# Performance work log

Measured on AMD Instinct MI355X. Metric: run time of the kernel, lower is better.

## Reference

```python
import jax, jax.numpy as jnp
import numpy as np

K_TOP = 2  # n_experts_per_tok
W_SCALE = 0.02  # keep activations numerically tame


def setup_inputs() -> dict:
    key = jax.random.key(0)
    ks = jax.random.split(key, 8)
    D, F, E = 1024, 1024, 8
    B, T = 4, 2048
    x = jax.random.normal(ks[0], (B, T, D), dtype=jnp.float32)
    router_w = jax.random.normal(ks[1], (D, E), dtype=jnp.float32) * W_SCALE
    sg = jax.random.normal(ks[2], (D, F), dtype=jnp.float32) * W_SCALE
    su = jax.random.normal(ks[3], (D, F), dtype=jnp.float32) * W_SCALE
    sd = jax.random.normal(ks[4], (F, D), dtype=jnp.float32) * W_SCALE
    wg = jax.random.normal(ks[5], (E, D, F), dtype=jnp.float32) * W_SCALE
    wu = jax.random.normal(ks[6], (E, D, F), dtype=jnp.float32) * W_SCALE
    wd = jax.random.normal(ks[7], (E, F, D), dtype=jnp.float32) * W_SCALE
    return {"x": x, "router_w": router_w, "sg": sg, "su": su, "sd": sd,
            "wg": wg, "wu": wu, "wd": wd}


def reference(x, router_w, sg, su, sd, wg, wu, wd):
    B, T, D = x.shape
    E = wg.shape[0]
    flat = x.reshape(-1, D)                       # [N, D]
    N = flat.shape[0]

    # shared SwiGLU expert (n_shared_experts = 1)
    shared = (jax.nn.silu(flat @ sg) * (flat @ su)) @ sd  # [N, D]

    # top-k softmax router with renormalization
    probs = jax.nn.softmax(flat @ router_w, axis=-1)      # [N, E]
    topk_p, topk_i = jax.lax.top_k(probs, K_TOP)          # [N, K]
    topk_p = topk_p / (jnp.sum(topk_p, axis=-1, keepdims=True) + 1e-9)

    # dense combine weights: scatter renormalized probs into [N, E]
    cw = jnp.zeros((N, E), dtype=flat.dtype).at[
        jnp.arange(N)[:, None], topk_i].add(topk_p)

    # per-expert SwiGLU on all tokens, weighted combine (jit-friendly MoE form)
    h = jax.nn.silu(jnp.einsum('nd,edf->nef', flat, wg)) \
        * jnp.einsum('nd,edf->nef', flat, wu)             # [N, E, F]
    eo = jnp.einsum('nef,efd->ned', h, wd)                # [N, E, D]
    routed = jnp.einsum('ned,ne->nd', eo, cw)             # [N, D]

    return (shared + routed).reshape(B, T, D)
```

## Files before the change

### kernel.cpp

```cpp
#include <hip/hip_runtime.h>

#define N_TOK    8192
#define D_DIM    1024
#define F_DIM    1024
#define NESH     9
#define MAX_RTD  18432
#define MAX_ROWS 26624
#define BM 256
#define BK 64
#define NK 16

#define MO 16
#define MT 25

typedef float  f4    __attribute__((ext_vector_type(4)));
typedef float  f32x4 __attribute__((ext_vector_type(4)));
typedef short  s16x8 __attribute__((ext_vector_type(8)));
typedef unsigned short u16x8 __attribute__((ext_vector_type(8)));
typedef unsigned short u16x4 __attribute__((ext_vector_type(4)));

static __device__ __forceinline__ unsigned short f2bf(float f) {
    union { float f; unsigned u; } v; v.f = f;
    unsigned r = v.u + 0x7FFFu + ((v.u >> 16) & 1u);
    return (unsigned short)(r >> 16);
}
static __device__ __forceinline__ float bf2f(unsigned short u) {
    union { unsigned u; float f; } v; v.u = ((unsigned)u) << 16; return v.f;
}

#define GLDS(gp, lp) __builtin_amdgcn_global_load_lds( \
    (const __attribute__((address_space(1))) void*)(gp), \
    (__attribute__((address_space(3))) void*)(lp), 16, 0, 0)

#define RSWZ(row, idx) ((idx) ^ (((row) & 7) << 3))

__global__ __launch_bounds__(256) void k_transpose(
    const float* __restrict__ wg, const float* __restrict__ wu,
    const float* __restrict__ wd, const float* __restrict__ sg,
    const float* __restrict__ su, const float* __restrict__ sd,
    unsigned short* __restrict__ wgt, unsigned short* __restrict__ wut,
    unsigned short* __restrict__ wdt)
{
    int bx = blockIdx.x;
    int m = bx >> 8;
    int tile = bx & 255;
    int ty = tile >> 4, tx = tile & 15;
    int set = m / 9, e = m % 9;
    const float* src; unsigned short* dst;
    if (set == 0)      { src = (e < 8) ? wg + (size_t)e*1048576 : sg; dst = wgt + (size_t)e*1048576; }
    else if (set == 1) { src = (e < 8) ? wu + (size_t)e*1048576 : su; dst = wut + (size_t)e*1048576; }
    else               { src = (e < 8) ? wd + (size_t)e*1048576 : sd; dst = wdt + (size_t)e*1048576; }

    __shared__ unsigned short ts[64 * 67];
    int t = threadIdx.x;
    int rT0 = ty * 64, cT0 = tx * 64;
    #pragma unroll
    for (int i = 0; i < 4; i++) {
        int idx = t + i * 256;
        int a  = idx >> 4;
        int b4 = (idx & 15) * 4;
        f4 v = *(const f4*)(src + (size_t)(cT0 + a) * 1024 + rT0 + b4);
        ts[a * 67 + b4 + 0] = f2bf(v[0]);
        ts[a * 67 + b4 + 1] = f2bf(v[1]);
        ts[a * 67 + b4 + 2] = f2bf(v[2]);
        ts[a * 67 + b4 + 3] = f2bf(v[3]);
    }
    __syncthreads();
    #pragma unroll
    for (int i = 0; i < 2; i++) {
        int slot = t + i * 256;
        int r  = slot >> 3;
        int c8 = (slot & 7) * 8;
        u16x8 o;
        #pragma unroll
        for (int k = 0; k < 8; k++) o[k] = ts[(c8 + k) * 67 + r];
        *(u16x8*)&dst[(size_t)(rT0 + r) * 1024 + cT0 + c8] = o;
    }
}

__global__ __launch_bounds__(256) void k_router(
    const float* __restrict__ x, const float* __restrict__ rw,
    unsigned short* __restrict__ xb,
    int* __restrict__ tk_i, float* __restrict__ tk_w)
{
    int wid = threadIdx.x >> 6, lane = threadIdx.x & 63;
    int n = blockIdx.x * 4 + wid;
    const float* xr = x + (size_t)n * D_DIM;
    unsigned short* xbr = xb + (size_t)n * D_DIM;
    float acc[8] = {0,0,0,0,0,0,0,0};
    #pragma unroll
    for (int it = 0; it < 4; it++) {
        int d0 = it * 256 + lane * 4;
        f4 xv = *(const f4*)(xr + d0);
        #pragma unroll
        for (int j = 0; j < 4; j++) {
            f4 r0 = *(const f4*)(rw + (size_t)(d0 + j) * 8);
            f4 r1 = *(const f4*)(rw + (size_t)(d0 + j) * 8 + 4);
            acc[0] += xv[j]*r0[0]; acc[1] += xv[j]*r0[1]; acc[2] += xv[j]*r0[2]; acc[3] += xv[j]*r0[3];
            acc[4] += xv[j]*r1[0]; acc[5] += xv[j]*r1[1]; acc[6] += xv[j]*r1[2]; acc[7] += xv[j]*r1[3];
        }
        u16x4 o; o[0]=f2bf(xv[0]); o[1]=f2bf(xv[1]); o[2]=f2bf(xv[2]); o[3]=f2bf(xv[3]);
        *(u16x4*)&xbr[d0] = o;
    }
    #pragma unroll
    for (int e = 0; e < 8; e++)
        for (int off = 32; off; off >>= 1)
            acc[e] += __shfl_xor(acc[e], off, 64);
    if (lane == 0) {
        float mx = acc[0];
        for (int e = 1; e < 8; e++) mx = fmaxf(mx, acc[e]);
        float p[8], s = 0.f;
        for (int e = 0; e < 8; e++) { p[e] = expf(acc[e] - mx); s += p[e]; }
        int i0 = 0;
        for (int e = 1; e < 8; e++) if (p[e] > p[i0]) i0 = e;
        int i1 = (i0 == 0) ? 1 : 0;
        for (int e = 0; e < 8; e++) if (e != i0 && p[e] > p[i1]) i1 = e;
        float p0 = p[i0] / s, p1 = p[i1] / s;
        float rs = p0 + p1 + 1e-9f;
        tk_i[2*n] = i0;  tk_i[2*n+1] = i1;
        tk_w[2*n] = p0 / rs;  tk_w[2*n+1] = p1 / rs;
    }
}

__global__ __launch_bounds__(1024) void k_count_scatter(
    const int* __restrict__ tk_i, const float* __restrict__ tk_w,
    int* __restrict__ meta,
    int* __restrict__ row_token, int* __restrict__ row_expert,
    int* __restrict__ tok_pos)
{
    __shared__ int cnt[1024 * 9];
    __shared__ int tot[8];
    __shared__ int off[9];
    const int t = threadIdx.x;
    const int lane = t & 63;
    const int wid = t >> 6;

    #pragma unroll
    for (int e = 0; e < 8; e++) cnt[t * 9 + e] = 0;
    __syncthreads();

    #pragma unroll
    for (int j = 0; j < 8; j++) {
        int n = t * 8 + j;
        cnt[t * 9 + tk_i[2 * n]]++;
        cnt[t * 9 + tk_i[2 * n + 1]]++;
    }
    __syncthreads();

    if (wid < 8) {
        const int e = wid;
        int carry = 0;
        for (int c = 0; c < 16; c++) {
            int i = c * 64 + lane;
            int v = cnt[i * 9 + e];
            int s = v;
            #pragma unroll
            for (int d = 1; d < 64; d <<= 1) {
                int u = __shfl_up(s, d, 64);
                if (lane >= d) s += u;
            }
            cnt[i * 9 + e] = s - v + carry;
            carry += __shfl(s, 63, 64);
        }
        if (lane == 0) tot[e] = carry;
    }
    __syncthreads();

    if (t == 0) {
        int acc = 0;
        #pragma unroll
        for (int e = 0; e < 8; e++) {
            off[e] = acc;
            meta[MO + e] = acc;
            acc += ((tot[e] + 255) >> 8) << 8;
        }
        off[8] = acc;
        meta[MO + 8] = acc;
        meta[MT] = acc + N_TOK;
    }
    __syncthreads();

    #pragma unroll
    for (int j = 0; j < 8; j++) {
        int n = t * 8 + j;
        #pragma unroll
        for (int k = 0; k < 2; k++) {
            int e = tk_i[2 * n + k];
            int pos = off[e] + cnt[t * 9 + e];
            cnt[t * 9 + e] = cnt[t * 9 + e] + 1;
            row_token[pos] = n; row_expert[pos] = e;
            tok_pos[2 * n + k] = pos;
        }
        int ps = off[8] + n;
        row_token[ps] = n; row_expert[ps] = 8;
    }
    #pragma unroll
    for (int e = 0; e < 8; e++) {
        int start = off[e] + tot[e], end = off[e + 1];
        for (int i = start + t; i < end; i += 1024) row_token[i] = -1;
    }
}

__global__ __launch_bounds__(512, 2) void k_gemm1(
    const unsigned short* __restrict__ xb,
    const unsigned short* __restrict__ wgt,
    const unsigned short* __restrict__ wut,
    const int* __restrict__ row_token,
    const int* __restrict__ row_expert,
    const int* __restrict__ meta,
    unsigned short* __restrict__ h)
{
    const int total = meta[MT];
    const int orig = blockIdx.x;
    const int bid = (orig & 7) * 104 + (orig >> 3);
    const int rt = bid >> 3, ct = bid & 7;
    const int row0 = rt * BM;
    if (row0 >= total) return;
    const int e = row_expert[row0];

    __shared__ __align__(16) unsigned short sA[2 * BM * BK];
    __shared__ __align__(16) unsigned short sBg[3 * 128 * BK];
    __shared__ __align__(16) unsigned short sBu[3 * 128 * BK];

    const int t = threadIdx.x;
    const int lane = t & 63;
    const int wid = t >> 6;
    const int wr = wid >> 1, wc = wid & 1;

    const unsigned short* asrc[4];
    #pragma unroll
    for (int i = 0; i < 4; i++) {
        int slot = t + i * 512;
        int row = slot >> 3;
        int cg  = (slot & 7) ^ (row & 7);
        int tok = row_token[row0 + row];
        if (tok < 0) tok = 0;
        asrc[i] = xb + (size_t)tok * D_DIM + cg * 8;
    }
    const unsigned short* bsrcg[2];
    const unsigned short* bsrcu[2];
    #pragma unroll
    for (int i = 0; i < 2; i++) {
        int slot = t + i * 512;
        int row = slot >> 3;
        int cg  = (slot & 7) ^ (row & 7);
        size_t off = ((size_t)e * F_DIM + ct * 128 + row) * D_DIM + cg * 8;
        bsrcg[i] = wgt + off;
        bsrcu[i] = wut + off;
    }

    f32x4 accg[4][4] = {}, accu[4][4] = {};

#define STAGE_A1(bb, k0) do { \
    unsigned short* dA = &sA[(bb) * (BM * BK)]; \
    _Pragma("unroll") \
    for (int i_ = 0; i_ < 4; i_++) GLDS(asrc[i_] + (k0), &dA[(t + i_ * 512) * 8]); \
    } while (0)
#define STAGE_B1(ss, k0) do { \
    unsigned short* dBg = &sBg[(ss) * (128 * BK)]; \
    unsigned short* dBu = &sBu[(ss) * (128 * BK)]; \
    _Pragma("unroll") \
    for (int i_ = 0; i_ < 2; i_++) { \
        GLDS(bsrcg[i_] + (k0), &dBg[(t + i_ * 512) * 8]); \
        GLDS(bsrcu[i_] + (k0), &dBu[(t + i_ * 512) * 8]); \
    } } while (0)

#define COMPUTE1(bb, ss) do { \
    const unsigned short* pA  = &sA[(bb) * (BM * BK)]; \
    const unsigned short* pBg = &sBg[(ss) * (128 * BK)]; \
    const unsigned short* pBu = &sBu[(ss) * (128 * BK)]; \
    _Pragma("unroll") \
    for (int kk = 0; kk < BK; kk += 32) { \
        const int koff = kk + (lane >> 4) * 8; \
        s16x8 a_[4], bg_[4], bu_[4]; \
        _Pragma("unroll") \
        for (int m_ = 0; m_ < 4; m_++) { \
            int row = wr * 64 + m_ * 16 + (lane & 15); \
            a_[m_] = *(const s16x8*)&pA[RSWZ(row, row * BK + koff)]; } \
        _Pragma("unroll") \
        for (int n_ = 0; n_ < 4; n_++) { \
            int row = wc * 64 + n_ * 16 + (lane & 15); \
            bg_[n_] = *(const s16x8*)&pBg[RSWZ(row, row * BK + koff)]; \
            bu_[n_] = *(const s16x8*)&pBu[RSWZ(row, row * BK + koff)]; } \
        _Pragma("unroll") \
        for (int m_ = 0; m_ < 4; m_++) \
            _Pragma("unroll") \
            for (int n_ = 0; n_ < 4; n_++) { \
                accg[m_][n_] = __builtin_amdgcn_mfma_f32_16x16x32_bf16(a_[m_], bg_[n_], accg[m_][n_], 0, 0, 0); \
                accu[m_][n_] = __builtin_amdgcn_mfma_f32_16x16x32_bf16(a_[m_], bu_[n_], accu[m_][n_], 0, 0, 0); } \
    } } while (0)

    STAGE_A1(0, 0);
    STAGE_B1(0, 0);
    STAGE_B1(1, BK);

    int sc = 0;
    int sst = 2;
    for (int u = 0; u < NK; u++) {
        if (u < NK - 1) STAGE_A1((u + 1) & 1, (u + 1) * BK);
        if (u < NK - 2) {
            STAGE_B1(sst, (u + 2) * BK);
            asm volatile("s_waitcnt vmcnt(12)" ::: "memory");
        } else if (u < NK - 1) {
            asm volatile("s_waitcnt vmcnt(8)" ::: "memory");
        } else {
            asm volatile("s_waitcnt vmcnt(0)" ::: "memory");
        }
        __builtin_amdgcn_s_barrier();
        __builtin_amdgcn_s_setprio(1);
        COMPUTE1(u & 1, sc);
        __builtin_amdgcn_s_setprio(0);
        asm volatile("" ::: "memory");
        __builtin_amdgcn_s_barrier();
        sc  = (sc  == 2) ? 0 : sc + 1;
        sst = (sst == 2) ? 0 : sst + 1;
    }

    #pragma unroll
    for (int m = 0; m < 4; m++)
        #pragma unroll
        for (int r = 0; r < 4; r++) {
            int grow = row0 + wr * 64 + m * 16 + (lane >> 4) * 4 + r;
            unsigned short* hrow = h + (size_t)grow * F_DIM + ct * 128 + wc * 64 + (lane & 15);
            #pragma unroll
            for (int n = 0; n < 4; n++) {
                float g = accg[m][n][r], u = accu[m][n][r];
                float sv = g / (1.f + __expf(-g));
                hrow[n * 16] = f2bf(sv * u);
            }
        }
#undef STAGE_A1
#undef STAGE_B1
#undef COMPUTE1
}

__global__ __launch_bounds__(512, 2) void k_gemm2(
    const unsigned short* __restrict__ h,
    const unsigned short* __restrict__ wdt,
    const int* __restrict__ row_expert,
    const int* __restrict__ meta,
    unsigned short* __restrict__ eo,
    float* __restrict__ out)
{
    const int total = meta[MT];
    const int off8 = meta[MO + 8];
    const int orig = blockIdx.x;
    const int bid = (orig & 7) * 52 + (orig >> 3);
    const int rt = bid >> 2, ct = bid & 3;
    const int row0 = rt * BM;
    if (row0 >= total) return;
    const int e = row_expert[row0];

    __shared__ __align__(16) unsigned short sA[2 * BM * BK];
    __shared__ __align__(16) unsigned short sB[3 * 256 * BK];

    const int t = threadIdx.x;
    const int lane = t & 63;
    const int wid = t >> 6;
    const int wr = wid >> 2, wc = wid & 3;

    const unsigned short* asrc[4];
    const unsigned short* bsrc[4];
    #pragma unroll
    for (int i = 0; i < 4; i++) {
        int slot = t + i * 512;
        int row = slot >> 3;
        int cg  = (slot & 7) ^ (row & 7);
        asrc[i] = h + (size_t)(row0 + row) * F_DIM + cg * 8;
        bsrc[i] = wdt + ((size_t)e * D_DIM + ct * 256 + row) * F_DIM + cg * 8;
    }

    f32x4 acc[8][4] = {};

#define STAGE_A2(bb, k0) do { \
    unsigned short* dA = &sA[(bb) * (BM * BK)]; \
    _Pragma("unroll") \
    for (int i_ = 0; i_ < 4; i_++) GLDS(asrc[i_] + (k0), &dA[(t + i_ * 512) * 8]); \
    } while (0)
#define STAGE_B2(ss, k0) do { \
    unsigned short* dB = &sB[(ss) * (256 * BK)]; \
    _Pragma("unroll") \
    for (int i_ = 0; i_ < 4; i_++) GLDS(bsrc[i_] + (k0), &dB[(t + i_ * 512) * 8]); \
    } while (0)

#define COMPUTE2(bb, ss) do { \
    const unsigned short* pA = &sA[(bb) * (BM * BK)]; \
    const unsigned short* pB = &sB[(ss) * (256 * BK)]; \
    _Pragma("unroll") \
    for (int kk = 0; kk < BK; kk += 32) { \
        const int koff = kk + (lane >> 4) * 8; \
        s16x8 a_[8], b_[4]; \
        _Pragma("unroll") \
        for (int m_ = 0; m_ < 8; m_++) { \
            int row = wr * 128 + m_ * 16 + (lane & 15); \
            a_[m_] = *(const s16x8*)&pA[RSWZ(row, row * BK + koff)]; } \
        _Pragma("unroll") \
        for (int n_ = 0; n_ < 4; n_++) { \
            int row = wc * 64 + n_ * 16 + (lane & 15); \
            b_[n_] = *(const s16x8*)&pB[RSWZ(row, row * BK + koff)]; } \
        _Pragma("unroll") \
        for (int m_ = 0; m_ < 8; m_++) \
            _Pragma("unroll") \
            for (int n_ = 0; n_ < 4; n_++) \
                acc[m_][n_] = __builtin_amdgcn_mfma_f32_16x16x32_bf16(a_[m_], b_[n_], acc[m_][n_], 0, 0, 0); \
    } } while (0)

    STAGE_A2(0, 0);
    STAGE_B2(0, 0);
    STAGE_B2(1, BK);

    int sc = 0, sst = 2;
    for (int u = 0; u < NK; u++) {
        if (u < NK - 1) STAGE_A2((u + 1) & 1, (u + 1) * BK);
        if (u < NK - 2) {
            STAGE_B2(sst, (u + 2) * BK);
            asm volatile("s_waitcnt vmcnt(12)" ::: "memory");
        } else if (u < NK - 1) {
            asm volatile("s_waitcnt vmcnt(8)" ::: "memory");
        } else {
            asm volatile("s_waitcnt vmcnt(0)" ::: "memory");
        }
        __builtin_amdgcn_s_barrier();
        __builtin_amdgcn_s_setprio(1);
        COMPUTE2(u & 1, sc);
        __builtin_amdgcn_s_setprio(0);
        asm volatile("" ::: "memory");
        __builtin_amdgcn_s_barrier();
        sc  = (sc  == 2) ? 0 : sc + 1;
        sst = (sst == 2) ? 0 : sst + 1;
    }

    if (e < 8) {
        #pragma unroll
        for (int mf = 0; mf < 8; mf++)
            #pragma unroll
            for (int r = 0; r < 4; r++) {
                int grow = row0 + wr * 128 + mf * 16 + (lane >> 4) * 4 + r;
                unsigned short* erow = eo + (size_t)grow * D_DIM + ct * 256 + wc * 64 + (lane & 15);
                #pragma unroll
                for (int ni = 0; ni < 4; ni++)
                    erow[ni * 16] = f2bf(acc[mf][ni][r]);
            }
    } else {
        #pragma unroll
        for (int mf = 0; mf < 8; mf++)
            #pragma unroll
            for (int r = 0; r < 4; r++) {
                int grow = row0 + wr * 128 + mf * 16 + (lane >> 4) * 4 + r;
                int tok = grow - off8;
                float* orow = out + (size_t)tok * D_DIM + ct * 256 + wc * 64 + (lane & 15);
                #pragma unroll
                for (int ni = 0; ni < 4; ni++)
                    orow[ni * 16] = acc[mf][ni][r];
            }
    }
#undef STAGE_A2
#undef STAGE_B2
#undef COMPUTE2
}

__global__ __launch_bounds__(256) void k_combine(
    const unsigned short* __restrict__ eo,
    const int* __restrict__ tok_pos, const float* __restrict__ tk_w,
    float* __restrict__ out)
{
    const int t = threadIdx.x;
    const int n = blockIdx.x * 2 + (t >> 7);
    const int c0 = (t & 127) * 8;
    const int p0 = tok_pos[2 * n], p1 = tok_pos[2 * n + 1];
    const float w0 = tk_w[2 * n], w1 = tk_w[2 * n + 1];
    u16x8 a = *(const u16x8*)&eo[(size_t)p0 * D_DIM + c0];
    u16x8 b = *(const u16x8*)&eo[(size_t)p1 * D_DIM + c0];
    float* orow = out + (size_t)n * D_DIM + c0;
    f4 o0 = *(f4*)orow, o1 = *(f4*)(orow + 4);
    #pragma unroll
    for (int j = 0; j < 4; j++) {
        o0[j] += w0 * bf2f(a[j])     + w1 * bf2f(b[j]);
        o1[j] += w0 * bf2f(a[4 + j]) + w1 * bf2f(b[4 + j]);
    }
    *(f4*)orow = o0;
    *(f4*)(orow + 4) = o1;
}

extern "C" void kernel_launch(void* const* d_in, const int* in_sizes, int n_in,
                              void* d_out, int out_size, void* d_ws, size_t ws_size,
                              hipStream_t stream)
{
    const float* x  = (const float*)d_in[0];
    const float* rw = (const float*)d_in[1];
    const float* sg = (const float*)d_in[2];
    const float* su = (const float*)d_in[3];
    const float* sd = (const float*)d_in[4];
    const float* wg = (const float*)d_in[5];
    const float* wu = (const float*)d_in[6];
    const float* wd = (const float*)d_in[7];
    float* out = (float*)d_out;

    char* p = (char*)d_ws;
    unsigned short* xb  = (unsigned short*)p; p += (size_t)N_TOK * D_DIM * 2;
    unsigned short* wgt = (unsigned short*)p; p += (size_t)NESH * D_DIM * F_DIM * 2;
    unsigned short* wut = (unsigned short*)p; p += (size_t)NESH * D_DIM * F_DIM * 2;
    unsigned short* wdt = (unsigned short*)p; p += (size_t)NESH * D_DIM * F_DIM * 2;
    unsigned short* h   = (unsigned short*)p; p += (size_t)MAX_ROWS * F_DIM * 2;
    int*   row_token  = (int*)p;   p += (size_t)MAX_ROWS * 4;
    int*   row_expert = (int*)p;   p += (size_t)MAX_ROWS * 4;
    int*   tok_pos = (int*)p;      p += (size_t)N_TOK * 2 * 4;
    int*   tk_i = (int*)p;         p += (size_t)N_TOK * 2 * 4;
    float* tk_w = (float*)p;       p += (size_t)N_TOK * 2 * 4;
    int*   meta = (int*)p;         p += 1024;
    if ((size_t)(p - (char*)d_ws) > ws_size) return;

    unsigned short* eo = wgt;

    k_router<<<N_TOK / 4, 256, 0, stream>>>(x, rw, xb, tk_i, tk_w);
    k_transpose<<<27 * 256, 256, 0, stream>>>(wg, wu, wd, sg, su, sd, wgt, wut, wdt);
    k_count_scatter<<<1, 1024, 0, stream>>>(tk_i, tk_w, meta, row_token, row_expert, tok_pos);
    k_gemm1<<<(MAX_ROWS / BM) * 8, 512, 0, stream>>>(xb, wgt, wut, row_token, row_expert, meta, h);
    k_gemm2<<<(MAX_ROWS / BM) * 4, 512, 0, stream>>>(h, wdt, row_expert, meta, eo, out);
    k_combine<<<N_TOK / 2, 256, 0, stream>>>(eo, tok_pos, tk_w, out);
}
```

Measured before the change: 323.5 us.

## Shrink grouped GEMM tiles to 128x128 with BK=32 and double buffering

Both expert GEMMs change from 256-row tiles with BK=64 and a triple-buffered B pipeline to 128x128 tiles with BK=32 and plain double buffering. The LDS swizzle is reworked for the narrower 32-wide K slice, launch bounds go to 4 blocks per CU, and expert padding drops from 256 to 128 rows. The goal is less padding waste and higher occupancy. In exchange, each tile does less arithmetic per byte loaded, runs twice as many K iterations with barriers, and has a shallower prefetch depth.

```diff
diff --git a/kernel.cpp b/kernel.cpp
--- a/kernel.cpp
+++ b/kernel.cpp
@@ -4,11 +4,11 @@
 #define D_DIM    1024
 #define F_DIM    1024
 #define NESH     9
-#define MAX_RTD  18432
+#define MAX_RTD  17408
 #define MAX_ROWS 26624
-#define BM 256
-#define BK 64
-#define NK 16
+#define BT 128
+#define BK 32
+#define NK 32
 
 #define MO 16
 #define MT 25
@@ -31,8 +31,6 @@
 #define GLDS(gp, lp) __builtin_amdgcn_global_load_lds( \
     (const __attribute__((address_space(1))) void*)(gp), \
     (__attribute__((address_space(3))) void*)(lp), 16, 0, 0)
-
-#define RSWZ(row, idx) ((idx) ^ (((row) & 7) << 3))
 
 __global__ __launch_bounds__(256) void k_transpose(
     const float* __restrict__ wg, const float* __restrict__ wu,
@@ -172,7 +170,7 @@
         for (int e = 0; e < 8; e++) {
             off[e] = acc;
             meta[MO + e] = acc;
-            acc += ((tot[e] + 255) >> 8) << 8;
+            acc += ((tot[e] + 127) >> 7) << 7;
         }
         off[8] = acc;
         meta[MO + 8] = acc;
@@ -201,7 +199,8 @@
     }
 }
 
-__global__ __launch_bounds__(512, 2) void k_gemm1(
+
+__global__ __launch_bounds__(512, 4) void k_gemm1(
     const unsigned short* __restrict__ xb,
     const unsigned short* __restrict__ wgt,
     const unsigned short* __restrict__ wut,
@@ -212,108 +211,75 @@
 {
     const int total = meta[MT];
     const int orig = blockIdx.x;
-    const int bid = (orig & 7) * 104 + (orig >> 3);
+    const int bid = (orig & 7) * 208 + (orig >> 3);
     const int rt = bid >> 3, ct = bid & 7;
-    const int row0 = rt * BM;
+    const int row0 = rt * BT;
     if (row0 >= total) return;
     const int e = row_expert[row0];
 
-    __shared__ __align__(16) unsigned short sA[2 * BM * BK];
-    __shared__ __align__(16) unsigned short sBg[3 * 128 * BK];
-    __shared__ __align__(16) unsigned short sBu[3 * 128 * BK];
+    __shared__ __align__(16) unsigned short sA[2 * 128 * 32];
+    __shared__ __align__(16) unsigned short sBg[2 * 128 * 32];
+    __shared__ __align__(16) unsigned short sBu[2 * 128 * 32];
 
     const int t = threadIdx.x;
     const int lane = t & 63;
+    const int lr = lane & 15;
+    const int kl = lane >> 4;
     const int wid = t >> 6;
-    const int wr = wid >> 1, wc = wid & 1;
-
-    const unsigned short* asrc[4];
-    #pragma unroll
-    for (int i = 0; i < 4; i++) {
-        int slot = t + i * 512;
-        int row = slot >> 3;
-        int cg  = (slot & 7) ^ (row & 7);
-        int tok = row_token[row0 + row];
-        if (tok < 0) tok = 0;
-        asrc[i] = xb + (size_t)tok * D_DIM + cg * 8;
-    }
-    const unsigned short* bsrcg[2];
-    const unsigned short* bsrcu[2];
-    #pragma unroll
-    for (int i = 0; i < 2; i++) {
-        int slot = t + i * 512;
-        int row = slot >> 3;
-        int cg  = (slot & 7) ^ (row & 7);
-        size_t off = ((size_t)e * F_DIM + ct * 128 + row) * D_DIM + cg * 8;
-        bsrcg[i] = wgt + off;
-        bsrcu[i] = wut + off;
-    }
-
-    f32x4 accg[4][4] = {}, accu[4][4] = {};
-
-#define STAGE_A1(bb, k0) do { \
-    unsigned short* dA = &sA[(bb) * (BM * BK)]; \
-    _Pragma("unroll") \
-    for (int i_ = 0; i_ < 4; i_++) GLDS(asrc[i_] + (k0), &dA[(t + i_ * 512) * 8]); \
+    const int wr = wid >> 2, wc = wid & 3;
+
+    const int srow = t >> 2;
+    const int scg  = (t & 3) ^ ((srow >> 1) & 3);
+    int tok = row_token[row0 + srow];
+    if (tok < 0) tok = 0;
+    const unsigned short* srcA = xb + (size_t)tok * D_DIM + scg * 8;
+    const unsigned short* srcG = wgt + ((size_t)e * F_DIM + ct * BT + srow) * D_DIM + scg * 8;
+    const unsigned short* srcU = wut + ((size_t)e * F_DIM + ct * BT + srow) * D_DIM + scg * 8;
+
+    f32x4 accg[4][2] = {}, accu[4][2] = {};
+
+#define ST1(bb, k0) do { \
+    GLDS(srcA + (k0), &sA[(bb) * 4096 + t * 8]); \
+    GLDS(srcG + (k0), &sBg[(bb) * 4096 + t * 8]); \
+    GLDS(srcU + (k0), &sBu[(bb) * 4096 + t * 8]); } while (0)
+
+#define COMPUTE1(bb) do { \
+    const unsigned short* pA  = &sA[(bb) * 4096]; \
+    const unsigned short* pG  = &sBg[(bb) * 4096]; \
+    const unsigned short* pU  = &sBu[(bb) * 4096]; \
+    s16x8 a_[4], g_[2], q_[2]; \
+    _Pragma("unroll") \
+    for (int m_ = 0; m_ < 4; m_++) { \
+        int row = wr * 64 + m_ * 16 + lr; \
+        a_[m_] = *(const s16x8*)&pA[row * 32 + ((kl ^ ((row >> 1) & 3)) << 3)]; } \
+    _Pragma("unroll") \
+    for (int n_ = 0; n_ < 2; n_++) { \
+        int row = wc * 32 + n_ * 16 + lr; \
+        int ix = row * 32 + ((kl ^ ((row >> 1) & 3)) << 3); \
+        g_[n_] = *(const s16x8*)&pG[ix]; \
+        q_[n_] = *(const s16x8*)&pU[ix]; } \
+    _Pragma("unroll") \
+    for (int m_ = 0; m_ < 4; m_++) \
+        _Pragma("unroll") \
+        for (int n_ = 0; n_ < 2; n_++) { \
+            accg[m_][n_] = __builtin_amdgcn_mfma_f32_16x16x32_bf16(a_[m_], g_[n_], accg[m_][n_], 0, 0, 0); \
+            accu[m_][n_] = __builtin_amdgcn_mfma_f32_16x16x32_bf16(a_[m_], q_[n_], accu[m_][n_], 0, 0, 0); } \
     } while (0)
-#define STAGE_B1(ss, k0) do { \
-    unsigned short* dBg = &sBg[(ss) * (128 * BK)]; \
-    unsigned short* dBu = &sBu[(ss) * (128 * BK)]; \
-    _Pragma("unroll") \
-    for (int i_ = 0; i_ < 2; i_++) { \
-        GLDS(bsrcg[i_] + (k0), &dBg[(t + i_ * 512) * 8]); \
-        GLDS(bsrcu[i_] + (k0), &dBu[(t + i_ * 512) * 8]); \
-    } } while (0)
-
-#define COMPUTE1(bb, ss) do { \
-    const unsigned short* pA  = &sA[(bb) * (BM * BK)]; \
-    const unsigned short* pBg = &sBg[(ss) * (128 * BK)]; \
-    const unsigned short* pBu = &sBu[(ss) * (128 * BK)]; \
-    _Pragma("unroll") \
-    for (int kk = 0; kk < BK; kk += 32) { \
-        const int koff = kk + (lane >> 4) * 8; \
-        s16x8 a_[4], bg_[4], bu_[4]; \
-        _Pragma("unroll") \
-        for (int m_ = 0; m_ < 4; m_++) { \
-            int row = wr * 64 + m_ * 16 + (lane & 15); \
-            a_[m_] = *(const s16x8*)&pA[RSWZ(row, row * BK + koff)]; } \
-        _Pragma("unroll") \
-        for (int n_ = 0; n_ < 4; n_++) { \
-            int row = wc * 64 + n_ * 16 + (lane & 15); \
-            bg_[n_] = *(const s16x8*)&pBg[RSWZ(row, row * BK + koff)]; \
-            bu_[n_] = *(const s16x8*)&pBu[RSWZ(row, row * BK + koff)]; } \
-        _Pragma("unroll") \
-        for (int m_ = 0; m_ < 4; m_++) \
-            _Pragma("unroll") \
-            for (int n_ = 0; n_ < 4; n_++) { \
-                accg[m_][n_] = __builtin_amdgcn_mfma_f32_16x16x32_bf16(a_[m_], bg_[n_], accg[m_][n_], 0, 0, 0); \
-                accu[m_][n_] = __builtin_amdgcn_mfma_f32_16x16x32_bf16(a_[m_], bu_[n_], accu[m_][n_], 0, 0, 0); } \
-    } } while (0)
-
-    STAGE_A1(0, 0);
-    STAGE_B1(0, 0);
-    STAGE_B1(1, BK);
-
-    int sc = 0;
-    int sst = 2;
+
+    ST1(0, 0);
     for (int u = 0; u < NK; u++) {
-        if (u < NK - 1) STAGE_A1((u + 1) & 1, (u + 1) * BK);
-        if (u < NK - 2) {
-            STAGE_B1(sst, (u + 2) * BK);
-            asm volatile("s_waitcnt vmcnt(12)" ::: "memory");
-        } else if (u < NK - 1) {
-            asm volatile("s_waitcnt vmcnt(8)" ::: "memory");
+        if (u < NK - 1) {
+            ST1((u + 1) & 1, (u + 1) * BK);
+            asm volatile("s_waitcnt vmcnt(3)" ::: "memory");
         } else {
             asm volatile("s_waitcnt vmcnt(0)" ::: "memory");
         }
         __builtin_amdgcn_s_barrier();
         __builtin_amdgcn_s_setprio(1);
-        COMPUTE1(u & 1, sc);
+        COMPUTE1(u & 1);
         __builtin_amdgcn_s_setprio(0);
         asm volatile("" ::: "memory");
         __builtin_amdgcn_s_barrier();
-        sc  = (sc  == 2) ? 0 : sc + 1;
-        sst = (sst == 2) ? 0 : sst + 1;
     }
 
     #pragma unroll
@@ -321,20 +287,19 @@
         #pragma unroll
         for (int r = 0; r < 4; r++) {
             int grow = row0 + wr * 64 + m * 16 + (lane >> 4) * 4 + r;
-            unsigned short* hrow = h + (size_t)grow * F_DIM + ct * 128 + wc * 64 + (lane & 15);
+            unsigned short* hrow = h + (size_t)grow * F_DIM + ct * BT + wc * 32 + lr;
             #pragma unroll
-            for (int n = 0; n < 4; n++) {
-                float g = accg[m][n][r], u = accu[m][n][r];
+            for (int n = 0; n < 2; n++) {
+                float g = accg[m][n][r], uu = accu[m][n][r];
                 float sv = g / (1.f + __expf(-g));
-                hrow[n * 16] = f2bf(sv * u);
+                hrow[n * 16] = f2bf(sv * uu);
             }
         }
-#undef STAGE_A1
-#undef STAGE_B1
+#undef ST1
 #undef COMPUTE1
 }
 
-__global__ __launch_bounds__(512, 2) void k_gemm2(
+__global__ __launch_bounds__(512, 4) void k_gemm2(
     const unsigned short* __restrict__ h,
     const unsigned short* __restrict__ wdt,
     const int* __restrict__ row_expert,
@@ -345,117 +310,93 @@
     const int total = meta[MT];
     const int off8 = meta[MO + 8];
     const int orig = blockIdx.x;
-    const int bid = (orig & 7) * 52 + (orig >> 3);
-    const int rt = bid >> 2, ct = bid & 3;
-    const int row0 = rt * BM;
+    const int bid = (orig & 7) * 208 + (orig >> 3);
+    const int rt = bid >> 3, ct = bid & 7;
+    const int row0 = rt * BT;
     if (row0 >= total) return;
     const int e = row_expert[row0];
 
-    __shared__ __align__(16) unsigned short sA[2 * BM * BK];
-    __shared__ __align__(16) unsigned short sB[3 * 256 * BK];
+    __shared__ __align__(16) unsigned short sA[2 * 128 * 32];
+    __shared__ __align__(16) unsigned short sB[2 * 128 * 32];
 
     const int t = threadIdx.x;
     const int lane = t & 63;
+    const int lr = lane & 15;
+    const int kl = lane >> 4;
     const int wid = t >> 6;
     const int wr = wid >> 2, wc = wid & 3;
 
-    const unsigned short* asrc[4];
-    const unsigned short* bsrc[4];
-    #pragma unroll
-    for (int i = 0; i < 4; i++) {
-        int slot = t + i * 512;
-        int row = slot >> 3;
-        int cg  = (slot & 7) ^ (row & 7);
-        asrc[i] = h + (size_t)(row0 + row) * F_DIM + cg * 8;
-        bsrc[i] = wdt + ((size_t)e * D_DIM + ct * 256 + row) * F_DIM + cg * 8;
-    }
-
-    f32x4 acc[8][4] = {};
-
-#define STAGE_A2(bb, k0) do { \
-    unsigned short* dA = &sA[(bb) * (BM * BK)]; \
-    _Pragma("unroll") \
-    for (int i_ = 0; i_ < 4; i_++) GLDS(asrc[i_] + (k0), &dA[(t + i_ * 512) * 8]); \
+    const int srow = t >> 2;
+    const int scg  = (t & 3) ^ ((srow >> 1) & 3);
+    const unsigned short* srcA = h + (size_t)(row0 + srow) * F_DIM + scg * 8;
+    const unsigned short* srcB = wdt + ((size_t)e * D_DIM + ct * BT + srow) * F_DIM + scg * 8;
+
+    f32x4 acc[4][2] = {};
+
+#define ST2(bb, k0) do { \
+    GLDS(srcA + (k0), &sA[(bb) * 4096 + t * 8]); \
+    GLDS(srcB + (k0), &sB[(bb) * 4096 + t * 8]); } while (0)
+
+#define COMPUTE2(bb) do { \
+    const unsigned short* pA = &sA[(bb) * 4096]; \
+    const unsigned short* pB = &sB[(bb) * 4096]; \
+    s16x8 a_[4], b_[2]; \
+    _Pragma("unroll") \
+    for (int m_ = 0; m_ < 4; m_++) { \
+        int row = wr * 64 + m_ * 16 + lr; \
+        a_[m_] = *(const s16x8*)&pA[row * 32 + ((kl ^ ((row >> 1) & 3)) << 3)]; } \
+    _Pragma("unroll") \
+    for (int n_ = 0; n_ < 2; n_++) { \
+        int row = wc * 32 + n_ * 16 + lr; \
+        b_[n_] = *(const s16x8*)&pB[row * 32 + ((kl ^ ((row >> 1) & 3)) << 3)]; } \
+    _Pragma("unroll") \
+    for (int m_ = 0; m_ < 4; m_++) \
+        _Pragma("unroll") \
+        for (int n_ = 0; n_ < 2; n_++) \
+            acc[m_][n_] = __builtin_amdgcn_mfma_f32_16x16x32_bf16(a_[m_], b_[n_], acc[m_][n_], 0, 0, 0); \
     } while (0)
-#define STAGE_B2(ss, k0) do { \
-    unsigned short* dB = &sB[(ss) * (256 * BK)]; \
-    _Pragma("unroll") \
-    for (int i_ = 0; i_ < 4; i_++) GLDS(bsrc[i_] + (k0), &dB[(t + i_ * 512) * 8]); \
-    } while (0)
-
-#define COMPUTE2(bb, ss) do { \
-    const unsigned short* pA = &sA[(bb) * (BM * BK)]; \
-    const unsigned short* pB = &sB[(ss) * (256 * BK)]; \
-    _Pragma("unroll") \
-    for (int kk = 0; kk < BK; kk += 32) { \
-        const int koff = kk + (lane >> 4) * 8; \
-        s16x8 a_[8], b_[4]; \
-        _Pragma("unroll") \
-        for (int m_ = 0; m_ < 8; m_++) { \
-            int row = wr * 128 + m_ * 16 + (lane & 15); \
-            a_[m_] = *(const s16x8*)&pA[RSWZ(row, row * BK + koff)]; } \
-        _Pragma("unroll") \
-        for (int n_ = 0; n_ < 4; n_++) { \
-            int row = wc * 64 + n_ * 16 + (lane & 15); \
-            b_[n_] = *(const s16x8*)&pB[RSWZ(row, row * BK + koff)]; } \
-        _Pragma("unroll") \
-        for (int m_ = 0; m_ < 8; m_++) \
-            _Pragma("unroll") \
-            for (int n_ = 0; n_ < 4; n_++) \
-                acc[m_][n_] = __builtin_amdgcn_mfma_f32_16x16x32_bf16(a_[m_], b_[n_], acc[m_][n_], 0, 0, 0); \
-    } } while (0)
-
-    STAGE_A2(0, 0);
-    STAGE_B2(0, 0);
-    STAGE_B2(1, BK);
-
-    int sc = 0, sst = 2;
+
+    ST2(0, 0);
     for (int u = 0; u < NK; u++) {
-        if (u < NK - 1) STAGE_A2((u + 1) & 1, (u + 1) * BK);
-        if (u < NK - 2) {
-            STAGE_B2(sst, (u + 2) * BK);
-            asm volatile("s_waitcnt vmcnt(12)" ::: "memory");
-        } else if (u < NK - 1) {
-            asm volatile("s_waitcnt vmcnt(8)" ::: "memory");
+        if (u < NK - 1) {
+            ST2((u + 1) & 1, (u + 1) * BK);
+            asm volatile("s_waitcnt vmcnt(2)" ::: "memory");
         } else {
             asm volatile("s_waitcnt vmcnt(0)" ::: "memory");
         }
         __builtin_amdgcn_s_barrier();
         __builtin_amdgcn_s_setprio(1);
-        COMPUTE2(u & 1, sc);
+        COMPUTE2(u & 1);
         __builtin_amdgcn_s_setprio(0);
         asm volatile("" ::: "memory");
         __builtin_amdgcn_s_barrier();
-        sc  = (sc  == 2) ? 0 : sc + 1;
-        sst = (sst == 2) ? 0 : sst + 1;
     }
 
     if (e < 8) {
         #pragma unroll
-        for (int mf = 0; mf < 8; mf++)
+        for (int m = 0; m < 4; m++)
             #pragma unroll
             for (int r = 0; r < 4; r++) {
-                int grow = row0 + wr * 128 + mf * 16 + (lane >> 4) * 4 + r;
-                unsigned short* erow = eo + (size_t)grow * D_DIM + ct * 256 + wc * 64 + (lane & 15);
+                int grow = row0 + wr * 64 + m * 16 + (lane >> 4) * 4 + r;
+                unsigned short* erow = eo + (size_t)grow * D_DIM + ct * BT + wc * 32 + lr;
                 #pragma unroll
-                for (int ni = 0; ni < 4; ni++)
-                    erow[ni * 16] = f2bf(acc[mf][ni][r]);
+                for (int n = 0; n < 2; n++)
+                    erow[n * 16] = f2bf(acc[m][n][r]);
             }
     } else {
         #pragma unroll
-        for (int mf = 0; mf < 8; mf++)
+        for (int m = 0; m < 4; m++)
             #pragma unroll
             for (int r = 0; r < 4; r++) {
-                int grow = row0 + wr * 128 + mf * 16 + (lane >> 4) * 4 + r;
+                int grow = row0 + wr * 64 + m * 16 + (lane >> 4) * 4 + r;
                 int tok = grow - off8;
-                float* orow = out + (size_t)tok * D_DIM + ct * 256 + wc * 64 + (lane & 15);
+                float* orow = out + (size_t)tok * D_DIM + ct * BT + wc * 32 + lr;
                 #pragma unroll
-                for (int ni = 0; ni < 4; ni++)
-                    orow[ni * 16] = acc[mf][ni][r];
+                for (int n = 0; n < 2; n++)
+                    orow[n * 16] = acc[m][n][r];
             }
     }
-#undef STAGE_A2
-#undef STAGE_B2
+#undef ST2
 #undef COMPUTE2
 }
 
@@ -515,7 +456,7 @@
     k_router<<<N_TOK / 4, 256, 0, stream>>>(x, rw, xb, tk_i, tk_w);
     k_transpose<<<27 * 256, 256, 0, stream>>>(wg, wu, wd, sg, su, sd, wgt, wut, wdt);
     k_count_scatter<<<1, 1024, 0, stream>>>(tk_i, tk_w, meta, row_token, row_expert, tok_pos);
-    k_gemm1<<<(MAX_ROWS / BM) * 8, 512, 0, stream>>>(xb, wgt, wut, row_token, row_expert, meta, h);
-    k_gemm2<<<(MAX_ROWS / BM) * 4, 512, 0, stream>>>(h, wdt, row_expert, meta, eo, out);
+    k_gemm1<<<(MAX_ROWS / BT) * 8, 512, 0, stream>>>(xb, wgt, wut, row_token, row_expert, meta, h);
+    k_gemm2<<<(MAX_ROWS / BT) * 8, 512, 0, stream>>>(h, wdt, row_expert, meta, eo, out);
     k_combine<<<N_TOK / 2, 256, 0, stream>>>(eo, tok_pos, tk_w, out);
 }
```

After: 317.3 us. About the same (-1.9%).
